# Performance work log

Measured on AMD Instinct MI355X. Metric: run time of the kernel, lower is better.

The kernel has to match this reference:

```python
import jax, jax.numpy as jnp
import numpy as np

G, N, D = 32, 2048, 128          # graphs, nodes per graph, feature dim
E_PER = 16384                     # edges per graph (avg degree 8)
E = G * E_PER
RATIO = 0.5
K = int(np.ceil(RATIO * N))       # nodes kept per graph = 1024


def setup_inputs() -> dict:
    key = jax.random.key(0)
    ks = jax.random.split(key, 8)
    x = jax.random.normal(ks[0], (G * N, D), dtype=jnp.float32)
    # random intra-graph edges, then offset into the global node index space
    src = jax.random.randint(ks[1], (G, E_PER), 0, N)
    dst = jax.random.randint(ks[2], (G, E_PER), 0, N)
    off = (jnp.arange(G) * N)[:, None]
    edge_index = jnp.stack([(src + off).reshape(-1), (dst + off).reshape(-1)]).astype(jnp.int32)
    batch = jnp.repeat(jnp.arange(G, dtype=jnp.int32), N)
    s = 1.0 / np.sqrt(D)
    w_rel = jax.random.normal(ks[3], (D,), dtype=jnp.float32) * s   # GraphConv lin_rel weight (out=1)
    b_rel = jnp.zeros((), dtype=jnp.float32)                         # GraphConv bias
    w_root = jax.random.normal(ks[4], (D,), dtype=jnp.float32) * s  # GraphConv lin_root (no bias)
    w_lin = jax.random.normal(ks[5], (D,), dtype=jnp.float32) * s   # nn.Linear(in_dim, 1)
    b_lin = jnp.zeros((), dtype=jnp.float32)
    return {"x": x, "edge_index": edge_index, "batch": batch,
            "w_rel": w_rel, "b_rel": b_rel, "w_root": w_root,
            "w_lin": w_lin, "b_lin": b_lin}


def reference(x, edge_index, batch, w_rel, b_rel, w_root, w_lin, b_lin):
    n_nodes = x.shape[0]
    src, dst = edge_index[0], edge_index[1]

    # score1 = GraphConv(x, edge_index): W_root x_i + W_rel * sum_{j->i} x_j + b
    agg = jax.ops.segment_sum(x[src], dst, num_segments=n_nodes)     # [n_nodes, D]
    score1 = agg @ w_rel + b_rel + x @ w_root                         # [n_nodes]
    # score2 = Linear(x)
    score2 = x @ w_lin + b_lin                                        # [n_nodes]
    # elementwise max over the two scores (torch.max over cat dim=1)
    score = jnp.maximum(score1, score2)

    # per-graph topk: batch is block-sorted with equal graph sizes
    _, idx = jax.lax.top_k(score.reshape(G, N), K)                    # [G, K] intra-graph idx
    perm = (idx + (jnp.arange(G) * N)[:, None]).reshape(-1)           # [G*K] global idx

    x_out = x[perm] * jnp.tanh(score[perm])[:, None]                  # [G*K, D]

    # filter_adj: keep edges whose endpoints both survive, re-index nodes.
    # Output edge count is data-dependent; we return a fixed-size reindexed
    # edge_index plus a validity mask (invalid edges set to 0).
    new_idx = jnp.full((n_nodes,), -1, dtype=edge_index.dtype)
    new_idx = new_idx.at[perm].set(jnp.arange(perm.shape[0], dtype=edge_index.dtype))
    ns, nd = new_idx[src], new_idx[dst]
    edge_mask = (ns >= 0) & (nd >= 0)
    new_edge_index = jnp.where(edge_mask, jnp.stack([ns, nd]), 0)

    new_batch = batch[perm]
    return (x_out, new_edge_index, edge_mask, new_batch)
```

## Files before the change

### kernel.cpp

```cpp
#include <hip/hip_runtime.h>
#include <hip/hip_bf16.h>

#define G_     32
#define N_     2048
#define D_     128
#define K_     1024
#define EPER_  16384

__global__ __launch_bounds__(256) void node_dots(
    const float* __restrict__ x,
    const float* __restrict__ w_rel,
    const float* __restrict__ w_root,
    const float* __restrict__ w_lin,
    const float* __restrict__ b_rel_p,
    const float* __restrict__ b_lin_p,
    float* __restrict__ p,
    float* __restrict__ base,
    float* __restrict__ s2,
    int n_nodes)
{
    int wave = (blockIdx.x * 256 + threadIdx.x) >> 6;
    int lane = threadIdx.x & 63;
    int node = wave * 2 + (lane >> 5);
    int c    = lane & 31;
    if (node >= n_nodes) return;

    float4 xv = ((const float4*)(x + (size_t)node * D_))[c];
    float4 wr = ((const float4*)w_rel)[c];
    float4 wo = ((const float4*)w_root)[c];
    float4 wl = ((const float4*)w_lin)[c];

    float pr = xv.x * wr.x + xv.y * wr.y + xv.z * wr.z + xv.w * wr.w;
    float po = xv.x * wo.x + xv.y * wo.y + xv.z * wo.z + xv.w * wo.w;
    float pl = xv.x * wl.x + xv.y * wl.y + xv.z * wl.z + xv.w * wl.w;

    #pragma unroll
    for (int off = 16; off; off >>= 1) {
        pr += __shfl_xor(pr, off);
        po += __shfl_xor(po, off);
        pl += __shfl_xor(pl, off);
    }
    if (c == 0) {
        p[node]    = pr;
        base[node] = po + b_rel_p[0];
        s2[node]   = pl + b_lin_p[0];
    }
}

__global__ __launch_bounds__(1024) void agg_partial(
    const int* __restrict__ src, const int* __restrict__ dst,
    const float* __restrict__ p, float* __restrict__ part)
{
    __shared__ float agg[N_];
    int g = blockIdx.x >> 3;
    int s = blockIdx.x & 7;
    agg[threadIdx.x]        = 0.0f;
    agg[threadIdx.x + 1024] = 0.0f;
    __syncthreads();

    int e0 = g * EPER_ + s * 2048 + threadIdx.x;
    int e1 = e0 + 1024;
    const float* gp = p + (size_t)g * N_;
    atomicAdd(&agg[dst[e0] & (N_ - 1)], gp[src[e0] & (N_ - 1)]);
    atomicAdd(&agg[dst[e1] & (N_ - 1)], gp[src[e1] & (N_ - 1)]);
    __syncthreads();

    float* op = part + ((size_t)g * 8 + s) * N_;
    op[threadIdx.x]        = agg[threadIdx.x];
    op[threadIdx.x + 1024] = agg[threadIdx.x + 1024];
}

__global__ __launch_bounds__(1024) void score_key(
    const float* __restrict__ part,
    const float* __restrict__ base, const float* __restrict__ s2,
    float* __restrict__ score, unsigned long long* __restrict__ keys)
{
    int node = blockIdx.x * 1024 + threadIdx.x;
    int g = node >> 11;
    int i = node & (N_ - 1);
    const float* pp = part + (size_t)g * 8 * N_ + i;
    float a = 0.0f;
    #pragma unroll
    for (int s = 0; s < 8; ++s) a += pp[(size_t)s * N_];
    float sc = fmaxf(base[node] + a, s2[node]);
    score[node] = sc;
    unsigned u = __float_as_uint(sc);
    u ^= ((int)u < 0) ? 0xFFFFFFFFu : 0x80000000u;
    keys[node] = ((unsigned long long)u << 32) | (unsigned)(N_ - 1 - i);
}

__global__ __launch_bounds__(1024) void topk_cnt(
    const unsigned long long* __restrict__ keys, int* __restrict__ cpart)
{
    int g  = blockIdx.x >> 3;
    int ib = (blockIdx.x >> 2) & 1;
    int jh = blockIdx.x & 3;
    const unsigned long long* gk = keys + (size_t)g * N_;
    int i = ib * 1024 + threadIdx.x;
    unsigned long long ki = gk[i];
    const unsigned long long* jk = gk + jh * 512;
    int c = 0;
    #pragma unroll 8
    for (int j = 0; j < 512; ++j) c += (jk[j] > ki) ? 1 : 0;
    cpart[((size_t)g * 4 + jh) * N_ + i] = c;
}

__global__ __launch_bounds__(256) void topk_merge(
    const int* __restrict__ cpart,
    int* __restrict__ new_idx, int* __restrict__ perm)
{
    int node = blockIdx.x * 256 + threadIdx.x;
    int g = node >> 11;
    int i = node & (N_ - 1);
    const int* cp = cpart + (size_t)g * 4 * N_ + i;
    int rank = cp[0] + cp[N_] + cp[2 * N_] + cp[3 * N_];
    if (rank < K_) {
        int pos = g * K_ + rank;
        perm[pos] = node;
        new_idx[node] = pos;
    } else {
        new_idx[node] = -1;
    }
}

__global__ __launch_bounds__(256) void gather_scale(
    const float* __restrict__ x, const float* __restrict__ score,
    const int* __restrict__ perm,
    float* __restrict__ out_x, float* __restrict__ out_b)
{
    int t   = blockIdx.x * 256 + threadIdx.x;
    int row = t >> 5;
    int c   = t & 31;
    int node = perm[row];
    float tz = tanhf(score[node]);
    float4 xv = ((const float4*)(x + (size_t)node * D_))[c];
    float4 v  = make_float4(xv.x * tz, xv.y * tz, xv.z * tz, xv.w * tz);
    ((float4*)(out_x + (size_t)row * D_))[c] = v;
    if (c == 0) out_b[row] = (float)(node >> 11);
}

__global__ __launch_bounds__(256) void edge_out_kernel(
    const int* __restrict__ src, const int* __restrict__ dst,
    const int* __restrict__ new_idx,
    float* __restrict__ out_e0,
    float* __restrict__ out_e1,
    float* __restrict__ out_m, int E)
{
    int e = blockIdx.x * 256 + threadIdx.x;
    if (e >= E) return;
    int ns = new_idx[src[e]];
    int nd = new_idx[dst[e]];
    bool m = (ns >= 0) && (nd >= 0);
    out_e0[e] = m ? (float)ns : 0.0f;
    out_e1[e] = m ? (float)nd : 0.0f;
    out_m[e]  = m ? 1.0f : 0.0f;
}

extern "C" void kernel_launch(void* const* d_in, const int* in_sizes, int n_in,
                              void* d_out, int out_size, void* d_ws, size_t ws_size,
                              hipStream_t stream)
{
    const float* x      = (const float*)d_in[0];
    const int*   ei     = (const int*)d_in[1];
    const float* w_rel  = (const float*)d_in[3];
    const float* b_rel  = (const float*)d_in[4];
    const float* w_root = (const float*)d_in[5];
    const float* w_lin  = (const float*)d_in[6];
    const float* b_lin  = (const float*)d_in[7];
    float* out = (float*)d_out;

    const int n_nodes = in_sizes[0] / D_;
    const int E       = in_sizes[1] / 2;
    const int* src = ei;
    const int* dst = ei + E;

    unsigned long long* keys = (unsigned long long*)d_ws;
    float* p     = (float*)(keys + n_nodes);
    float* base  = p + n_nodes;
    float* s2    = base + n_nodes;
    float* score = s2 + n_nodes;
    float* part  = score + n_nodes;
    int*   cpart = (int*)(part + (size_t)G_ * 8 * N_);
    int*   new_idx = cpart + (size_t)G_ * 4 * N_;
    int*   perm    = new_idx + n_nodes;

    const size_t offEI = (size_t)G_ * K_ * D_;
    const size_t offM  = offEI + 2 * (size_t)E;
    const size_t offB  = offM + (size_t)E;

    node_dots<<<n_nodes / 8, 256, 0, stream>>>(
        x, w_rel, w_root, w_lin, b_rel, b_lin, p, base, s2, n_nodes);
    agg_partial<<<G_ * 8, 1024, 0, stream>>>(src, dst, p, part);
    score_key<<<n_nodes / 1024, 1024, 0, stream>>>(part, base, s2, score, keys);
    topk_cnt<<<G_ * 8, 1024, 0, stream>>>(keys, cpart);
    topk_merge<<<n_nodes / 256, 256, 0, stream>>>(cpart, new_idx, perm);
    gather_scale<<<(G_ * K_ * 32) / 256, 256, 0, stream>>>(
        x, score, perm, out, out + offB);
    edge_out_kernel<<<(E + 255) / 256, 256, 0, stream>>>(
        src, dst, new_idx, out + offEI, out + offEI + E, out + offM, E);
}
```

Measured before the change: 132.2 us.

## Fuse score, rank-count and merge into one LDS top-k kernel; merge gather and edge kernels

Score/key computation, the pairwise rank count and the rank merge are folded into one kernel per graph slice. The keys live in shared memory and four lanes split each node's comparisons, combining their counts with shuffles. The gather-scale and edge-filter kernels are also merged into a single launch with block-range dispatch. This cuts four launches and the global round trips for keys and partial counts, at the cost of each of the 8 blocks per graph recomputing all 2048 scores redundantly.

Result: faster. 121.8 us (-7.8%).

```diff
diff --git a/kernel.cpp b/kernel.cpp
--- a/kernel.cpp
+++ b/kernel.cpp
@@ -70,90 +70,86 @@
     op[threadIdx.x + 1024] = agg[threadIdx.x + 1024];
 }
 
-__global__ __launch_bounds__(1024) void score_key(
+__global__ __launch_bounds__(1024) void topk_fused(
     const float* __restrict__ part,
     const float* __restrict__ base, const float* __restrict__ s2,
-    float* __restrict__ score, unsigned long long* __restrict__ keys)
+    float* __restrict__ score,
+    int* __restrict__ new_idx, int* __restrict__ perm)
 {
-    int node = blockIdx.x * 1024 + threadIdx.x;
-    int g = node >> 11;
-    int i = node & (N_ - 1);
-    const float* pp = part + (size_t)g * 8 * N_ + i;
-    float a = 0.0f;
-    #pragma unroll
-    for (int s = 0; s < 8; ++s) a += pp[(size_t)s * N_];
-    float sc = fmaxf(base[node] + a, s2[node]);
-    score[node] = sc;
-    unsigned u = __float_as_uint(sc);
-    u ^= ((int)u < 0) ? 0xFFFFFFFFu : 0x80000000u;
-    keys[node] = ((unsigned long long)u << 32) | (unsigned)(N_ - 1 - i);
-}
+    __shared__ unsigned long long keys[N_];
+    int g  = blockIdx.x >> 3;
+    int ib = blockIdx.x & 7;
 
-__global__ __launch_bounds__(1024) void topk_cnt(
-    const unsigned long long* __restrict__ keys, int* __restrict__ cpart)
-{
-    int g  = blockIdx.x >> 3;
-    int ib = (blockIdx.x >> 2) & 1;
-    int jh = blockIdx.x & 3;
-    const unsigned long long* gk = keys + (size_t)g * N_;
-    int i = ib * 1024 + threadIdx.x;
-    unsigned long long ki = gk[i];
-    const unsigned long long* jk = gk + jh * 512;
+    for (int i = threadIdx.x; i < N_; i += 1024) {
+        const float* pp = part + (size_t)g * 8 * N_ + i;
+        float a = 0.0f;
+        #pragma unroll
+        for (int s = 0; s < 8; ++s) a += pp[(size_t)s * N_];
+        int node = g * N_ + i;
+        float sc = fmaxf(base[node] + a, s2[node]);
+        if (ib == 0) score[node] = sc;
+        unsigned u = __float_as_uint(sc);
+        u ^= ((int)u < 0) ? 0xFFFFFFFFu : 0x80000000u;
+        keys[i] = ((unsigned long long)u << 32) | (unsigned)(N_ - 1 - i);
+    }
+    __syncthreads();
+
+    int il = threadIdx.x >> 2;
+    int q  = threadIdx.x & 3;
+    int i  = ib * 256 + il;
+    unsigned long long ki = keys[i];
+
+    const ulonglong2* k2 = (const ulonglong2*)keys + q * 256;
     int c = 0;
     #pragma unroll 8
-    for (int j = 0; j < 512; ++j) c += (jk[j] > ki) ? 1 : 0;
-    cpart[((size_t)g * 4 + jh) * N_ + i] = c;
-}
-
-__global__ __launch_bounds__(256) void topk_merge(
-    const int* __restrict__ cpart,
-    int* __restrict__ new_idx, int* __restrict__ perm)
-{
-    int node = blockIdx.x * 256 + threadIdx.x;
-    int g = node >> 11;
-    int i = node & (N_ - 1);
-    const int* cp = cpart + (size_t)g * 4 * N_ + i;
-    int rank = cp[0] + cp[N_] + cp[2 * N_] + cp[3 * N_];
-    if (rank < K_) {
-        int pos = g * K_ + rank;
-        perm[pos] = node;
-        new_idx[node] = pos;
-    } else {
-        new_idx[node] = -1;
+    for (int j = 0; j < 256; ++j) {
+        ulonglong2 kk = k2[(j + q) & 255];
+        c += (kk.x > ki) + (kk.y > ki);
+    }
+    c += __shfl_xor(c, 1);
+    c += __shfl_xor(c, 2);
+    if (q == 0) {
+        int node = g * N_ + i;
+        if (c < K_) {
+            int pos = g * K_ + c;
+            perm[pos] = node;
+            new_idx[node] = pos;
+        } else {
+            new_idx[node] = -1;
+        }
     }
 }
 
-__global__ __launch_bounds__(256) void gather_scale(
+__global__ __launch_bounds__(256) void gather_edge(
     const float* __restrict__ x, const float* __restrict__ score,
-    const int* __restrict__ perm,
-    float* __restrict__ out_x, float* __restrict__ out_b)
-{
-    int t   = blockIdx.x * 256 + threadIdx.x;
-    int row = t >> 5;
-    int c   = t & 31;
-    int node = perm[row];
-    float tz = tanhf(score[node]);
-    float4 xv = ((const float4*)(x + (size_t)node * D_))[c];
-    float4 v  = make_float4(xv.x * tz, xv.y * tz, xv.z * tz, xv.w * tz);
-    ((float4*)(out_x + (size_t)row * D_))[c] = v;
-    if (c == 0) out_b[row] = (float)(node >> 11);
-}
-
-__global__ __launch_bounds__(256) void edge_out_kernel(
+    const int* __restrict__ perm, const int* __restrict__ new_idx,
     const int* __restrict__ src, const int* __restrict__ dst,
-    const int* __restrict__ new_idx,
-    float* __restrict__ out_e0,
-    float* __restrict__ out_e1,
+    float* __restrict__ out_x, float* __restrict__ out_b,
+    float* __restrict__ out_e0, float* __restrict__ out_e1,
     float* __restrict__ out_m, int E)
 {
-    int e = blockIdx.x * 256 + threadIdx.x;
-    if (e >= E) return;
-    int ns = new_idx[src[e]];
-    int nd = new_idx[dst[e]];
-    bool m = (ns >= 0) && (nd >= 0);
-    out_e0[e] = m ? (float)ns : 0.0f;
-    out_e1[e] = m ? (float)nd : 0.0f;
-    out_m[e]  = m ? 1.0f : 0.0f;
+    int b = blockIdx.x;
+    if (b < 4096) {
+        int t   = b * 256 + threadIdx.x;
+        int row = t >> 5;
+        int c   = t & 31;
+        int node = perm[row];
+        float tz = tanhf(score[node]);
+        float4 xv = ((const float4*)(x + (size_t)node * D_))[c];
+        ((float4*)(out_x + (size_t)row * D_))[c] =
+            make_float4(xv.x * tz, xv.y * tz, xv.z * tz, xv.w * tz);
+        if (c == 0) out_b[row] = (float)(node >> 11);
+    } else {
+        int e = (b - 4096) * 256 + threadIdx.x;
+        if (e < E) {
+            int ns = new_idx[src[e]];
+            int nd = new_idx[dst[e]];
+            bool m = (ns >= 0) && (nd >= 0);
+            out_e0[e] = m ? (float)ns : 0.0f;
+            out_e1[e] = m ? (float)nd : 0.0f;
+            out_m[e]  = m ? 1.0f : 0.0f;
+        }
+    }
 }
 
 extern "C" void kernel_launch(void* const* d_in, const int* in_sizes, int n_in,
@@ -174,14 +170,12 @@
     const int* src = ei;
     const int* dst = ei + E;
 
-    unsigned long long* keys = (unsigned long long*)d_ws;
-    float* p     = (float*)(keys + n_nodes);
+    float* p     = (float*)d_ws;
     float* base  = p + n_nodes;
     float* s2    = base + n_nodes;
     float* score = s2 + n_nodes;
     float* part  = score + n_nodes;
-    int*   cpart = (int*)(part + (size_t)G_ * 8 * N_);
-    int*   new_idx = cpart + (size_t)G_ * 4 * N_;
+    int*   new_idx = (int*)(part + (size_t)G_ * 8 * N_);
     int*   perm    = new_idx + n_nodes;
 
     const size_t offEI = (size_t)G_ * K_ * D_;
@@ -191,11 +185,8 @@
     node_dots<<<n_nodes / 8, 256, 0, stream>>>(
         x, w_rel, w_root, w_lin, b_rel, b_lin, p, base, s2, n_nodes);
     agg_partial<<<G_ * 8, 1024, 0, stream>>>(src, dst, p, part);
-    score_key<<<n_nodes / 1024, 1024, 0, stream>>>(part, base, s2, score, keys);
-    topk_cnt<<<G_ * 8, 1024, 0, stream>>>(keys, cpart);
-    topk_merge<<<n_nodes / 256, 256, 0, stream>>>(cpart, new_idx, perm);
-    gather_scale<<<(G_ * K_ * 32) / 256, 256, 0, stream>>>(
-        x, score, perm, out, out + offB);
-    edge_out_kernel<<<(E + 255) / 256, 256, 0, stream>>>(
-        src, dst, new_idx, out + offEI, out + offEI + E, out + offM, E);
+    topk_fused<<<G_ * 8, 1024, 0, stream>>>(part, base, s2, score, new_idx, perm);
+    gather_edge<<<4096 + 2048, 256, 0, stream>>>(
+        x, score, perm, new_idx, src, dst,
+        out, out + offB, out + offEI, out + offEI + E, out + offM, E);
 }
```

## Fuse score, top-k rank counting, and gather-scale into one kernel

Applied to the files above, without the earlier changes.

Four kernels (score/key build, pairwise rank count, merge, gather-scale) are merged into one kernel per graph slice. Each block recomputes the full graph's keys in shared memory, register-tiles four candidates per thread for the pairwise comparisons, and accumulates ranks with shared atomics. It then scatters the surviving rows straight from registers and removes the global keys, cpart and perm buffers. This cuts three launches and their global round-trips, at the cost of every one of the 8 blocks per graph redundantly recomputing that graph's scores.

New measurement: 120.7 us. 8.7% less time.

```diff
diff --git a/kernel.cpp b/kernel.cpp
--- a/kernel.cpp
+++ b/kernel.cpp
@@ -1,5 +1,4 @@
 #include <hip/hip_runtime.h>
-#include <hip/hip_bf16.h>
 
 #define G_     32
 #define N_     2048
@@ -70,73 +69,85 @@
     op[threadIdx.x + 1024] = agg[threadIdx.x + 1024];
 }
 
-__global__ __launch_bounds__(1024) void score_key(
+__global__ __launch_bounds__(1024) void topk_gather(
     const float* __restrict__ part,
     const float* __restrict__ base, const float* __restrict__ s2,
-    float* __restrict__ score, unsigned long long* __restrict__ keys)
-{
-    int node = blockIdx.x * 1024 + threadIdx.x;
-    int g = node >> 11;
-    int i = node & (N_ - 1);
-    const float* pp = part + (size_t)g * 8 * N_ + i;
-    float a = 0.0f;
-    #pragma unroll
-    for (int s = 0; s < 8; ++s) a += pp[(size_t)s * N_];
-    float sc = fmaxf(base[node] + a, s2[node]);
-    score[node] = sc;
-    unsigned u = __float_as_uint(sc);
-    u ^= ((int)u < 0) ? 0xFFFFFFFFu : 0x80000000u;
-    keys[node] = ((unsigned long long)u << 32) | (unsigned)(N_ - 1 - i);
-}
-
-__global__ __launch_bounds__(1024) void topk_cnt(
-    const unsigned long long* __restrict__ keys, int* __restrict__ cpart)
-{
-    int g  = blockIdx.x >> 3;
-    int ib = (blockIdx.x >> 2) & 1;
-    int jh = blockIdx.x & 3;
-    const unsigned long long* gk = keys + (size_t)g * N_;
-    int i = ib * 1024 + threadIdx.x;
-    unsigned long long ki = gk[i];
-    const unsigned long long* jk = gk + jh * 512;
-    int c = 0;
-    #pragma unroll 8
-    for (int j = 0; j < 512; ++j) c += (jk[j] > ki) ? 1 : 0;
-    cpart[((size_t)g * 4 + jh) * N_ + i] = c;
-}
-
-__global__ __launch_bounds__(256) void topk_merge(
-    const int* __restrict__ cpart,
-    int* __restrict__ new_idx, int* __restrict__ perm)
-{
-    int node = blockIdx.x * 256 + threadIdx.x;
-    int g = node >> 11;
-    int i = node & (N_ - 1);
-    const int* cp = cpart + (size_t)g * 4 * N_ + i;
-    int rank = cp[0] + cp[N_] + cp[2 * N_] + cp[3 * N_];
-    if (rank < K_) {
-        int pos = g * K_ + rank;
-        perm[pos] = node;
-        new_idx[node] = pos;
-    } else {
-        new_idx[node] = -1;
-    }
-}
-
-__global__ __launch_bounds__(256) void gather_scale(
-    const float* __restrict__ x, const float* __restrict__ score,
-    const int* __restrict__ perm,
+    const float* __restrict__ x,
+    int* __restrict__ new_idx,
     float* __restrict__ out_x, float* __restrict__ out_b)
 {
-    int t   = blockIdx.x * 256 + threadIdx.x;
-    int row = t >> 5;
-    int c   = t & 31;
-    int node = perm[row];
-    float tz = tanhf(score[node]);
-    float4 xv = ((const float4*)(x + (size_t)node * D_))[c];
-    float4 v  = make_float4(xv.x * tz, xv.y * tz, xv.z * tz, xv.w * tz);
-    ((float4*)(out_x + (size_t)row * D_))[c] = v;
-    if (c == 0) out_b[row] = (float)(node >> 11);
+    __shared__ unsigned long long keys_s[N_];
+    __shared__ int   cnt_s[256];
+    __shared__ float sc_s[256];
+    const int tid = threadIdx.x;
+    const int g   = blockIdx.x >> 3;
+    const int sb  = blockIdx.x & 7;
+
+    for (int i = tid; i < N_; i += 1024) {
+        const float* pp = part + (size_t)g * 8 * N_ + i;
+        float a = 0.0f;
+        #pragma unroll
+        for (int s = 0; s < 8; ++s) a += pp[(size_t)s * N_];
+        int node = g * N_ + i;
+        float sc = fmaxf(base[node] + a, s2[node]);
+        if ((i >> 8) == sb) sc_s[i & 255] = sc;
+        unsigned u = __float_as_uint(sc);
+        u ^= ((int)u < 0) ? 0xFFFFFFFFu : 0x80000000u;
+        keys_s[i] = ((unsigned long long)u << 32) | (unsigned)(N_ - 1 - i);
+    }
+    if (tid < 256) cnt_s[tid] = 0;
+    __syncthreads();
+
+    {
+        int iq = tid & 63;
+        int js = tid >> 6;
+        int ibase = sb * 256 + iq * 4;
+        unsigned long long ki0 = keys_s[ibase + 0];
+        unsigned long long ki1 = keys_s[ibase + 1];
+        unsigned long long ki2 = keys_s[ibase + 2];
+        unsigned long long ki3 = keys_s[ibase + 3];
+        const ulonglong2* k2 = (const ulonglong2*)keys_s + js * 64;
+        int c0 = 0, c1 = 0, c2 = 0, c3 = 0;
+        #pragma unroll 8
+        for (int j = 0; j < 64; ++j) {
+            ulonglong2 kk = k2[j];
+            c0 += (kk.x > ki0) + (kk.y > ki0);
+            c1 += (kk.x > ki1) + (kk.y > ki1);
+            c2 += (kk.x > ki2) + (kk.y > ki2);
+            c3 += (kk.x > ki3) + (kk.y > ki3);
+        }
+        atomicAdd(&cnt_s[iq * 4 + 0], c0);
+        atomicAdd(&cnt_s[iq * 4 + 1], c1);
+        atomicAdd(&cnt_s[iq * 4 + 2], c2);
+        atomicAdd(&cnt_s[iq * 4 + 3], c3);
+    }
+    __syncthreads();
+
+    if (tid < 256) {
+        int rank = cnt_s[tid];
+        int node = g * N_ + sb * 256 + tid;
+        new_idx[node] = (rank < K_) ? (g * K_ + rank) : -1;
+    }
+    __syncthreads();
+
+    {
+        int grp = tid >> 5;
+        int l32 = tid & 31;
+        #pragma unroll
+        for (int it = 0; it < 8; ++it) {
+            int s = it * 32 + grp;
+            int rank = cnt_s[s];
+            if (rank < K_) {
+                int node = g * N_ + sb * 256 + s;
+                int row  = g * K_ + rank;
+                float tz = tanhf(sc_s[s]);
+                float4 xv = ((const float4*)(x + (size_t)node * D_))[l32];
+                ((float4*)(out_x + (size_t)row * D_))[l32] =
+                    make_float4(xv.x * tz, xv.y * tz, xv.z * tz, xv.w * tz);
+                if (l32 == 0) out_b[row] = (float)g;
+            }
+        }
+    }
 }
 
 __global__ __launch_bounds__(256) void edge_out_kernel(
@@ -174,15 +185,11 @@
     const int* src = ei;
     const int* dst = ei + E;
 
-    unsigned long long* keys = (unsigned long long*)d_ws;
-    float* p     = (float*)(keys + n_nodes);
+    float* p     = (float*)d_ws;
     float* base  = p + n_nodes;
     float* s2    = base + n_nodes;
-    float* score = s2 + n_nodes;
-    float* part  = score + n_nodes;
-    int*   cpart = (int*)(part + (size_t)G_ * 8 * N_);
-    int*   new_idx = cpart + (size_t)G_ * 4 * N_;
-    int*   perm    = new_idx + n_nodes;
+    float* part  = s2 + n_nodes;
+    int*   new_idx = (int*)(part + (size_t)G_ * 8 * N_);
 
     const size_t offEI = (size_t)G_ * K_ * D_;
     const size_t offM  = offEI + 2 * (size_t)E;
@@ -191,11 +198,8 @@
     node_dots<<<n_nodes / 8, 256, 0, stream>>>(
         x, w_rel, w_root, w_lin, b_rel, b_lin, p, base, s2, n_nodes);
     agg_partial<<<G_ * 8, 1024, 0, stream>>>(src, dst, p, part);
-    score_key<<<n_nodes / 1024, 1024, 0, stream>>>(part, base, s2, score, keys);
-    topk_cnt<<<G_ * 8, 1024, 0, stream>>>(keys, cpart);
-    topk_merge<<<n_nodes / 256, 256, 0, stream>>>(cpart, new_idx, perm);
-    gather_scale<<<(G_ * K_ * 32) / 256, 256, 0, stream>>>(
-        x, score, perm, out, out + offB);
+    topk_gather<<<G_ * 8, 1024, 0, stream>>>(
+        part, base, s2, x, new_idx, out, out + offB);
     edge_out_kernel<<<(E + 255) / 256, 256, 0, stream>>>(
         src, dst, new_idx, out + offEI, out + offEI + E, out + offM, E);
 }
```
